# Kernel tuning notes

Hardware: AMD Instinct MI355X
Metric: run time of the kernel (lower is better)

## Reference

```python
import jax, jax.numpy as jnp
import numpy as np

NUM_GRAPHS = 512


def _sage_conv(x, src, tgt, num_nodes, w_n, b_n, w_r):
    # PyG SAGEConv with mean aggregation:
    #   out = mean_{j in N(i)} x_j @ w_n + b_n + x_i @ w_r
    msgs = x[src]                                   # [E, d] gather
    agg = jax.ops.segment_sum(msgs, tgt, num_segments=num_nodes)   # [N, d]
    deg = jax.ops.segment_sum(jnp.ones((src.shape[0],), x.dtype), tgt,
                              num_segments=num_nodes)              # [N]
    agg = agg / jnp.maximum(deg, 1.0)[:, None]
    return agg @ w_n + b_n + x @ w_r


def setup_inputs() -> dict:
    key = jax.random.key(0)
    ks = jax.random.split(key, 10)
    N, E, D_IN, D_H, D_OUT = 50000, 800000, 128, 128, 10
    s = 0.05
    x = jax.random.normal(ks[0], (N, D_IN), dtype=jnp.float32)
    edge_index = jax.random.randint(ks[1], (2, E), 0, N, dtype=jnp.int64)
    batch = jnp.sort(jax.random.randint(ks[2], (N,), 0, NUM_GRAPHS, dtype=jnp.int64))
    return {
        "x": x,
        "edge_index": edge_index,
        "batch": batch,
        "w1_n": jax.random.normal(ks[3], (D_IN, D_H), dtype=jnp.float32) * s,
        "b1": jnp.zeros((D_H,), jnp.float32),
        "w1_r": jax.random.normal(ks[4], (D_IN, D_H), dtype=jnp.float32) * s,
        "w2_n": jax.random.normal(ks[5], (D_H, D_H), dtype=jnp.float32) * s,
        "b2": jnp.zeros((D_H,), jnp.float32),
        "w2_r": jax.random.normal(ks[6], (D_H, D_H), dtype=jnp.float32) * s,
        "fc_w": jax.random.normal(ks[7], (D_H, D_OUT), dtype=jnp.float32) * s,
        "fc_b": jnp.zeros((D_OUT,), jnp.float32),
    }


def reference(x, edge_index, batch, w1_n, b1, w1_r, w2_n, b2, w2_r, fc_w, fc_b):
    N = x.shape[0]
    src, tgt = edge_index[0], edge_index[1]
    h = _sage_conv(x, src, tgt, N, w1_n, b1, w1_r)
    h = jax.nn.relu(h)  # dropout is identity in eval mode
    h = _sage_conv(h, src, tgt, N, w2_n, b2, w2_r)
    # global_mean_pool over graph ids
    pooled = jax.ops.segment_sum(h, batch, num_segments=NUM_GRAPHS)
    cnt = jax.ops.segment_sum(jnp.ones((N,), h.dtype), batch, num_segments=NUM_GRAPHS)
    pooled = pooled / jnp.maximum(cnt, 1.0)[:, None]
    return pooled @ fc_w + fc_b
```

## Files before the change

kernel.cpp:

```cpp
#include <hip/hip_runtime.h>

#define D 128
#define G_NUM 512

typedef unsigned short u16;
typedef unsigned int u32;
typedef __attribute__((ext_vector_type(8))) short bf16x8;
typedef __attribute__((ext_vector_type(4))) float f32x4;

__device__ __forceinline__ float bf2f(u16 u) { return __uint_as_float(((u32)u) << 16); }
__device__ __forceinline__ u16 f2bf_rne(float f) {
    u32 u = __float_as_uint(f);
    return (u16)((u + 0x7FFFu + ((u >> 16) & 1u)) >> 16);
}
__device__ __forceinline__ u32 packf(float v) {
    u16 h = f2bf_rne(v);
    u16 l = f2bf_rne(v - bf2f(h));
    return ((u32)h << 16) | l;
}
__device__ __forceinline__ float pk_hi(u32 u) { return __uint_as_float(u & 0xFFFF0000u); }
__device__ __forceinline__ float pk_lo(u32 u) { return __uint_as_float(u << 16); }

__device__ __forceinline__ void unpack8(const u32* w, bf16x8& hi, bf16x8& lo) {
    union { u32 u[4]; bf16x8 v; } H, L;
#pragma unroll
    for (int p = 0; p < 4; p++) {
        u32 a = w[2 * p], b = w[2 * p + 1];
        H.u[p] = (b & 0xFFFF0000u) | (a >> 16);
        L.u[p] = (b << 16) | (a & 0xFFFFu);
    }
    hi = H.v;
    lo = L.v;
}

__global__ void prep_kernel(const float* __restrict__ x, u32* __restrict__ xp,
                            const float* __restrict__ w0, const float* __restrict__ w1,
                            const float* __restrict__ w2, const float* __restrict__ w3,
                            u16* __restrict__ wp,
                            const int* __restrict__ batch, int* __restrict__ gstart,
                            const int* __restrict__ tgt, int* __restrict__ deg,
                            int n4, int E, int N, int NBX, int NBE) {
    int b = blockIdx.x, t = threadIdx.x;
    if (b < NBX) {
        int i = b * 256 + t;
        if (i >= n4) return;
        float4 v = ((const float4*)x)[i];
        uint4 o;
        o.x = packf(v.x);
        o.y = packf(v.y);
        o.z = packf(v.z);
        o.w = packf(v.w);
        ((uint4*)xp)[i] = o;
    } else if (b < NBX + NBE) {
        int e = (b - NBX) * 256 + t;
        if (e < E) atomicAdd(&deg[tgt[e]], 1);
    } else if (b < NBX + NBE + 32) {
        int id = (b - NBX - NBE) * 256 + t;
        int g = id & 3, c = (id >> 2) & 127, kt = (id >> 9) & 3, mat = id >> 11;
        const float* W = (mat == 0) ? w0 : (mat == 1) ? w1 : (mat == 2) ? w2 : w3;
        u16* dh = wp + mat * 32768 + ((size_t)(kt * 128 + c) * 4 + g) * 8;
        u16* dl = dh + 16384;
#pragma unroll
        for (int j = 0; j < 8; j++) {
            float v = W[(size_t)(kt * 32 + g * 8 + j) * D + c];
            u16 h = f2bf_rne(v);
            dh[j] = h;
            dl[j] = f2bf_rne(v - bf2f(h));
        }
    } else {
        int i = (b - NBX - NBE - 32) * 256 + t;
        if (i >= N) return;
        int bb = batch[i];
        int bp = (i == 0) ? -1 : batch[i - 1];
        for (int g = bp + 1; g <= bb; g++) gstart[g] = i;
        if (i == N - 1)
            for (int g = bb + 1; g <= G_NUM; g++) gstart[g] = N;
    }
}

__global__ void scan1_kernel(const int* __restrict__ deg, int* __restrict__ row_excl,
                             int* __restrict__ partial, int N) {
    __shared__ int s[256];
    int t = threadIdx.x, i = blockIdx.x * 256 + t;
    int v = (i < N) ? deg[i] : 0;
    s[t] = v;
    __syncthreads();
    for (int off = 1; off < 256; off <<= 1) {
        int add = (t >= off) ? s[t - off] : 0;
        __syncthreads();
        s[t] += add;
        __syncthreads();
    }
    if (i < N) row_excl[i] = s[t] - v;
    if (t == 255) partial[blockIdx.x] = s[255];
}

__global__ void scan2_kernel(int* __restrict__ partial, int NB) {
    __shared__ int s[256];
    int t = threadIdx.x;
    int v = (t < NB) ? partial[t] : 0;
    s[t] = v;
    __syncthreads();
    for (int off = 1; off < 256; off <<= 1) {
        int add = (t >= off) ? s[t - off] : 0;
        __syncthreads();
        s[t] += add;
        __syncthreads();
    }
    if (t < NB) partial[t] = s[t] - v;
}

__global__ void scan3_kernel(int* __restrict__ row_start, const int* __restrict__ partial,
                             int* __restrict__ deg, float* __restrict__ rdeg, int N, int E) {
    int i = blockIdx.x * blockDim.x + threadIdx.x;
    if (i < N) {
        row_start[i] += partial[blockIdx.x];
        float d = (float)deg[i];
        rdeg[i] = 1.0f / fmaxf(d, 1.0f);
        deg[i] = 0;
    }
    if (i == 0) row_start[N] = E;
}

__global__ void fill_kernel(const int* __restrict__ src, const int* __restrict__ tgt,
                            const int* __restrict__ row_start, int* __restrict__ cursor,
                            int* __restrict__ col_idx, int E) {
    int e = blockIdx.x * blockDim.x + threadIdx.x;
    if (e >= E) return;
    int t = tgt[e];
    int pos = row_start[t] + atomicAdd(&cursor[t], 1);
    col_idx[pos] = src[e];
}

template <int LAYER>
__global__ __launch_bounds__(512, 4) void sage_fused_kernel(
    const int* __restrict__ row_start, const int* __restrict__ col_idx,
    const float* __restrict__ rdeg, const u32* __restrict__ feat_pk,
    const u16* __restrict__ Wnh, const u16* __restrict__ Wnl,
    const u16* __restrict__ Wrh, const u16* __restrict__ Wrl,
    const float* __restrict__ bias, u32* __restrict__ out_pk,
    float* __restrict__ out_f32, int N, int NT) {
    __shared__ u32 agg[16 * 132];

    int tid = threadIdx.x;
    int lane = tid & 63;
    int wave = tid >> 6;
    int r = lane & 15, g = lane >> 4;

    bf16x8 Bn[4][2], Br[4][2];
#pragma unroll
    for (int kt = 0; kt < 4; kt++) {
        size_t wo = ((size_t)(kt * 128 + r) * 4 + g) * 8 + (size_t)wave * 512;
        Bn[kt][0] = *(const bf16x8*)(Wnh + wo);
        Bn[kt][1] = *(const bf16x8*)(Wnl + wo);
        Br[kt][0] = *(const bf16x8*)(Wrh + wo);
        Br[kt][1] = *(const bf16x8*)(Wrl + wo);
    }
    float bv = bias[wave * 16 + r];

    int nl = tid >> 5;
    int q = tid & 31;

    for (int rt = blockIdx.x; rt < NT; rt += gridDim.x) {
        int node = rt * 16 + nl;
        float ax = 0.f, ay = 0.f, az = 0.f, aw = 0.f;
        if (node < N) {
            int beg = row_start[node], end = row_start[node + 1];
            int i = beg;
            for (; i + 4 <= end; i += 4) {
                int s0 = col_idx[i], s1 = col_idx[i + 1], s2 = col_idx[i + 2], s3 = col_idx[i + 3];
                uint4 v0 = ((const uint4*)feat_pk)[(size_t)s0 * 32 + q];
                uint4 v1 = ((const uint4*)feat_pk)[(size_t)s1 * 32 + q];
                uint4 v2 = ((const uint4*)feat_pk)[(size_t)s2 * 32 + q];
                uint4 v3 = ((const uint4*)feat_pk)[(size_t)s3 * 32 + q];
                ax += (pk_hi(v0.x) + pk_lo(v0.x)) + (pk_hi(v1.x) + pk_lo(v1.x)) +
                      (pk_hi(v2.x) + pk_lo(v2.x)) + (pk_hi(v3.x) + pk_lo(v3.x));
                ay += (pk_hi(v0.y) + pk_lo(v0.y)) + (pk_hi(v1.y) + pk_lo(v1.y)) +
                      (pk_hi(v2.y) + pk_lo(v2.y)) + (pk_hi(v3.y) + pk_lo(v3.y));
                az += (pk_hi(v0.z) + pk_lo(v0.z)) + (pk_hi(v1.z) + pk_lo(v1.z)) +
                      (pk_hi(v2.z) + pk_lo(v2.z)) + (pk_hi(v3.z) + pk_lo(v3.z));
                aw += (pk_hi(v0.w) + pk_lo(v0.w)) + (pk_hi(v1.w) + pk_lo(v1.w)) +
                      (pk_hi(v2.w) + pk_lo(v2.w)) + (pk_hi(v3.w) + pk_lo(v3.w));
            }
            for (; i < end; i++) {
                int s = col_idx[i];
                uint4 v = ((const uint4*)feat_pk)[(size_t)s * 32 + q];
                ax += pk_hi(v.x) + pk_lo(v.x);
                ay += pk_hi(v.y) + pk_lo(v.y);
                az += pk_hi(v.z) + pk_lo(v.z);
                aw += pk_hi(v.w) + pk_lo(v.w);
            }
            float rd = rdeg[node];
            ax *= rd; ay *= rd; az *= rd; aw *= rd;
        }
        uint4 pk4;
        pk4.x = packf(ax);
        pk4.y = packf(ay);
        pk4.z = packf(az);
        pk4.w = packf(aw);
        *(uint4*)&agg[nl * 132 + q * 4] = pk4;
        __syncthreads();

        int grow = min(rt * 16 + r, N - 1);
        const u32* xrow = feat_pk + (size_t)grow * D;
        f32x4 acc = (f32x4){0.f, 0.f, 0.f, 0.f};
#pragma unroll
        for (int kt = 0; kt < 4; kt++) {
            u32 awb[8];
            *(uint4*)&awb[0] = *(const uint4*)&agg[r * 132 + kt * 32 + g * 8];
            *(uint4*)&awb[4] = *(const uint4*)&agg[r * 132 + kt * 32 + g * 8 + 4];
            bf16x8 ah, al;
            unpack8(awb, ah, al);
            u32 xwb[8];
            *(uint4*)&xwb[0] = *(const uint4*)(xrow + kt * 32 + g * 8);
            *(uint4*)&xwb[4] = *(const uint4*)(xrow + kt * 32 + g * 8 + 4);
            bf16x8 xh, xl;
            unpack8(xwb, xh, xl);
            acc = __builtin_amdgcn_mfma_f32_16x16x32_bf16(ah, Bn[kt][0], acc, 0, 0, 0);
            acc = __builtin_amdgcn_mfma_f32_16x16x32_bf16(al, Bn[kt][0], acc, 0, 0, 0);
            acc = __builtin_amdgcn_mfma_f32_16x16x32_bf16(ah, Bn[kt][1], acc, 0, 0, 0);
            acc = __builtin_amdgcn_mfma_f32_16x16x32_bf16(xh, Br[kt][0], acc, 0, 0, 0);
            acc = __builtin_amdgcn_mfma_f32_16x16x32_bf16(xl, Br[kt][0], acc, 0, 0, 0);
            acc = __builtin_amdgcn_mfma_f32_16x16x32_bf16(xh, Br[kt][1], acc, 0, 0, 0);
        }
#pragma unroll
        for (int reg = 0; reg < 4; reg++) {
            int row = rt * 16 + g * 4 + reg;
            if (row >= N) continue;
            float v = acc[reg] + bv;
            if (LAYER == 0) {
                v = fmaxf(v, 0.f);
                out_pk[(size_t)row * D + wave * 16 + r] = packf(v);
            } else {
                out_f32[(size_t)row * D + wave * 16 + r] = v;
            }
        }
        __syncthreads();
    }
}

__global__ __launch_bounds__(128) void pool_fc_kernel(
    const float* __restrict__ h2, const int* __restrict__ gstart,
    const float* __restrict__ fcw, const float* __restrict__ fcb, float* __restrict__ out) {
    __shared__ float p[D];
    int g = blockIdx.x, t = threadIdx.x;
    int s = gstart[g], e = gstart[g + 1];
    float acc = 0.f;
    for (int r = s; r < e; r++) acc += h2[(size_t)r * D + t];
    float rc = 1.0f / fmaxf((float)(e - s), 1.0f);
    p[t] = acc * rc;
    __syncthreads();
    if (t < 10) {
        float o = fcb[t];
#pragma unroll
        for (int k = 0; k < D; k++) o += p[k] * fcw[k * 10 + t];
        out[g * 10 + t] = o;
    }
}

extern "C" void kernel_launch(void* const* d_in, const int* in_sizes, int n_in,
                              void* d_out, int out_size, void* d_ws, size_t ws_size,
                              hipStream_t stream) {
    const float* x   = (const float*)d_in[0];
    const int*   ei  = (const int*)d_in[1];
    const int* batch = (const int*)d_in[2];
    const float* w1n = (const float*)d_in[3];
    const float* b1  = (const float*)d_in[4];
    const float* w1r = (const float*)d_in[5];
    const float* w2n = (const float*)d_in[6];
    const float* b2  = (const float*)d_in[7];
    const float* w2r = (const float*)d_in[8];
    const float* fcw = (const float*)d_in[9];
    const float* fcb = (const float*)d_in[10];
    float* out = (float*)d_out;

    int N = in_sizes[0] / D;
    int E = in_sizes[1] / 2;
    const int* src = ei;
    const int* tgt = ei + E;
    int NB = (N + 255) / 256;

    auto au = [](size_t v) { return (v + 255) & ~(size_t)255; };
    char* p = (char*)d_ws;
    int*   deg       = (int*)p;    p += au((size_t)N * 4);
    int*   row_start = (int*)p;    p += au((size_t)(N + 1) * 4);
    int*   partial   = (int*)p;    p += au(256 * 4);
    int*   col_idx   = (int*)p;    p += au((size_t)E * 4);
    float* rdeg      = (float*)p;  p += au((size_t)N * 4);
    int*   gstart    = (int*)p;    p += au((size_t)(G_NUM + 1) * 4);
    u16*   wp        = (u16*)p;    p += au((size_t)8 * 16384 * 2);
    u32*   xp        = (u32*)p;    p += au((size_t)N * D * 4);
    u32*   h1p       = (u32*)p;    p += au((size_t)N * D * 4);
    float* h2        = (float*)xp;

    hipMemsetAsync(deg, 0, (size_t)N * 4, stream);

    int n4 = N * 32;
    int NBX = (n4 + 255) / 256;
    int NBE = (E + 255) / 256;
    prep_kernel<<<NBX + NBE + 32 + NB, 256, 0, stream>>>(
        x, xp, w1n, w1r, w2n, w2r, wp, batch, gstart, tgt, deg, n4, E, N, NBX, NBE);

    scan1_kernel<<<NB, 256, 0, stream>>>(deg, row_start, partial, N);
    scan2_kernel<<<1, 256, 0, stream>>>(partial, NB);
    scan3_kernel<<<NB, 256, 0, stream>>>(row_start, partial, deg, rdeg, N, E);
    fill_kernel<<<NBE, 256, 0, stream>>>(src, tgt, row_start, deg, col_idx, E);

    int NT = (N + 15) / 16;
    int grid = NT < 512 ? NT : 512;

    sage_fused_kernel<0><<<grid, 512, 0, stream>>>(
        row_start, col_idx, rdeg, xp,
        wp + 0 * 32768, wp + 0 * 32768 + 16384,
        wp + 1 * 32768, wp + 1 * 32768 + 16384,
        b1, h1p, nullptr, N, NT);

    sage_fused_kernel<1><<<grid, 512, 0, stream>>>(
        row_start, col_idx, rdeg, h1p,
        wp + 2 * 32768, wp + 2 * 32768 + 16384,
        wp + 3 * 32768, wp + 3 * 32768 + 16384,
        b2, nullptr, h2, N, NT);

    pool_fc_kernel<<<G_NUM, 128, 0, stream>>>(h2, gstart, fcw, fcb, out);
}
```

Baseline: 370.6 us.

## Merge scan kernels into decoupled lookback, widen pooling, double fused grid

The three-kernel degree scan becomes a single-pass scan. Blocks take ordered tickets and use decoupled lookback flags to get their prefix, which removes two launches and the partial-sum round trip. The pooling kernel now uses 512 threads with float4 row-parallel loads and a shared-memory tree reduction instead of one serial row loop per column. The grid cap for the fused SAGE kernels rises from 512 to 1024 blocks. The lookback spins on flags and so relies on forward progress across blocks, and the workspace memset now also has to clear the ticket and flags.

```diff
diff --git a/kernel.cpp b/kernel.cpp
--- a/kernel.cpp
+++ b/kernel.cpp
@@ -78,10 +78,17 @@
     }
 }
 
-__global__ void scan1_kernel(const int* __restrict__ deg, int* __restrict__ row_excl,
-                             int* __restrict__ partial, int N) {
+__global__ __launch_bounds__(256) void scan_kernel(
+    int* __restrict__ deg, int* __restrict__ row_start, float* __restrict__ rdeg,
+    int* __restrict__ ticket, int* __restrict__ bflag, int* __restrict__ bstate,
+    int N, int E) {
     __shared__ int s[256];
-    int t = threadIdx.x, i = blockIdx.x * 256 + t;
+    __shared__ int sblk, sprev;
+    int t = threadIdx.x;
+    if (t == 0) sblk = atomicAdd(ticket, 1);
+    __syncthreads();
+    int b = sblk;
+    int i = b * 256 + t;
     int v = (i < N) ? deg[i] : 0;
     s[t] = v;
     __syncthreads();
@@ -91,35 +98,31 @@
         s[t] += add;
         __syncthreads();
     }
-    if (i < N) row_excl[i] = s[t] - v;
-    if (t == 255) partial[blockIdx.x] = s[255];
-}
-
-__global__ void scan2_kernel(int* __restrict__ partial, int NB) {
-    __shared__ int s[256];
-    int t = threadIdx.x;
-    int v = (t < NB) ? partial[t] : 0;
-    s[t] = v;
+    int incl = s[t];
+    int total = s[255];
+    if (t == 0) {
+        atomicExch(&bstate[2 * b], total);
+        __threadfence();
+        atomicExch(&bflag[b], 1);
+        int excl = 0;
+        for (int p = b - 1; p >= 0; --p) {
+            int f;
+            do { f = atomicAdd(&bflag[p], 0); } while (f == 0);
+            if (f == 2) { excl += atomicAdd(&bstate[2 * p + 1], 0); break; }
+            excl += atomicAdd(&bstate[2 * p], 0);
+        }
+        sprev = excl;
+        atomicExch(&bstate[2 * b + 1], excl + total);
+        __threadfence();
+        atomicExch(&bflag[b], 2);
+    }
     __syncthreads();
-    for (int off = 1; off < 256; off <<= 1) {
-        int add = (t >= off) ? s[t - off] : 0;
-        __syncthreads();
-        s[t] += add;
-        __syncthreads();
-    }
-    if (t < NB) partial[t] = s[t] - v;
-}
-
-__global__ void scan3_kernel(int* __restrict__ row_start, const int* __restrict__ partial,
-                             int* __restrict__ deg, float* __restrict__ rdeg, int N, int E) {
-    int i = blockIdx.x * blockDim.x + threadIdx.x;
     if (i < N) {
-        row_start[i] += partial[blockIdx.x];
-        float d = (float)deg[i];
-        rdeg[i] = 1.0f / fmaxf(d, 1.0f);
+        row_start[i] = sprev + incl - v;
+        rdeg[i] = 1.0f / fmaxf((float)v, 1.0f);
         deg[i] = 0;
     }
-    if (i == 0) row_start[N] = E;
+    if (b == 0 && t == 0) row_start[N] = E;
 }
 
 __global__ void fill_kernel(const int* __restrict__ src, const int* __restrict__ tgt,
@@ -239,21 +242,35 @@
     }
 }
 
-__global__ __launch_bounds__(128) void pool_fc_kernel(
+__global__ __launch_bounds__(512) void pool_fc_kernel(
     const float* __restrict__ h2, const int* __restrict__ gstart,
     const float* __restrict__ fcw, const float* __restrict__ fcb, float* __restrict__ out) {
-    __shared__ float p[D];
+    __shared__ float red[16][132];
     int g = blockIdx.x, t = threadIdx.x;
     int s = gstart[g], e = gstart[g + 1];
-    float acc = 0.f;
-    for (int r = s; r < e; r++) acc += h2[(size_t)r * D + t];
-    float rc = 1.0f / fmaxf((float)(e - s), 1.0f);
-    p[t] = acc * rc;
+    int rr = t >> 5, c4 = t & 31;
+    float4 acc = {0.f, 0.f, 0.f, 0.f};
+    for (int r = s + rr; r < e; r += 16) {
+        float4 v = ((const float4*)(h2 + (size_t)r * D))[c4];
+        acc.x += v.x; acc.y += v.y; acc.z += v.z; acc.w += v.w;
+    }
+    *(float4*)&red[rr][c4 * 4] = acc;
     __syncthreads();
+#pragma unroll
+    for (int off = 8; off >= 1; off >>= 1) {
+        if (rr < off) {
+            float4 a = *(float4*)&red[rr][c4 * 4];
+            float4 b = *(float4*)&red[rr + off][c4 * 4];
+            a.x += b.x; a.y += b.y; a.z += b.z; a.w += b.w;
+            *(float4*)&red[rr][c4 * 4] = a;
+        }
+        __syncthreads();
+    }
     if (t < 10) {
+        float rc = 1.0f / fmaxf((float)(e - s), 1.0f);
         float o = fcb[t];
 #pragma unroll
-        for (int k = 0; k < D; k++) o += p[k] * fcw[k * 10 + t];
+        for (int k = 0; k < D; k++) o += red[0][k] * rc * fcw[k * 10 + t];
         out[g * 10 + t] = o;
     }
 }
@@ -283,8 +300,10 @@
     auto au = [](size_t v) { return (v + 255) & ~(size_t)255; };
     char* p = (char*)d_ws;
     int*   deg       = (int*)p;    p += au((size_t)N * 4);
+    int*   ticket    = (int*)p;    p += au(4);
+    int*   bflag     = (int*)p;    p += au((size_t)NB * 4);
+    int*   bstate    = (int*)p;    p += au((size_t)2 * NB * 4);
     int*   row_start = (int*)p;    p += au((size_t)(N + 1) * 4);
-    int*   partial   = (int*)p;    p += au(256 * 4);
     int*   col_idx   = (int*)p;    p += au((size_t)E * 4);
     float* rdeg      = (float*)p;  p += au((size_t)N * 4);
     int*   gstart    = (int*)p;    p += au((size_t)(G_NUM + 1) * 4);
@@ -293,7 +312,8 @@
     u32*   h1p       = (u32*)p;    p += au((size_t)N * D * 4);
     float* h2        = (float*)xp;
 
-    hipMemsetAsync(deg, 0, (size_t)N * 4, stream);
+    size_t zbytes = (size_t)((char*)(bflag + NB) - (char*)deg);
+    hipMemsetAsync(deg, 0, zbytes, stream);
 
     int n4 = N * 32;
     int NBX = (n4 + 255) / 256;
@@ -301,13 +321,11 @@
     prep_kernel<<<NBX + NBE + 32 + NB, 256, 0, stream>>>(
         x, xp, w1n, w1r, w2n, w2r, wp, batch, gstart, tgt, deg, n4, E, N, NBX, NBE);
 
-    scan1_kernel<<<NB, 256, 0, stream>>>(deg, row_start, partial, N);
-    scan2_kernel<<<1, 256, 0, stream>>>(partial, NB);
-    scan3_kernel<<<NB, 256, 0, stream>>>(row_start, partial, deg, rdeg, N, E);
+    scan_kernel<<<NB, 256, 0, stream>>>(deg, row_start, rdeg, ticket, bflag, bstate, N, E);
     fill_kernel<<<NBE, 256, 0, stream>>>(src, tgt, row_start, deg, col_idx, E);
 
     int NT = (N + 15) / 16;
-    int grid = NT < 512 ? NT : 512;
+    int grid = NT < 1024 ? NT : 1024;
 
     sage_fused_kernel<0><<<grid, 512, 0, stream>>>(
         row_start, col_idx, rdeg, xp,
@@ -321,5 +339,5 @@
         wp + 3 * 32768, wp + 3 * 32768 + 16384,
         b2, nullptr, h2, N, NT);
 
-    pool_fc_kernel<<<G_NUM, 128, 0, stream>>>(h2, gstart, fcw, fcb, out);
-}
+    pool_fc_kernel<<<G_NUM, 512, 0, stream>>>(h2, gstart, fcw, fcb, out);
+}
```

After: 376.6 us. Within noise of the previous version (+1.6%).
